# Kernel optimization log

Hardware: AMD Instinct MI355X
Metric: run time of the kernel (lower is better)

Reference implementation:

```python
import jax, jax.numpy as jnp
import numpy as np

HIDDEN = 1024
NUM_HEADS = 16
HEAD_DIM = HIDDEN // NUM_HEADS


def setup_inputs() -> dict:
    key = jax.random.key(0)
    ks = jax.random.split(key, 13)
    B, S, H = 4, 2048, HIDDEN
    sc = 1.0 / np.sqrt(H)
    inp = {
        'queries': jax.random.normal(ks[0], (B, S, H), jnp.float32),
        'keys': jax.random.normal(ks[1], (B, S, H), jnp.float32),
        'values': jax.random.normal(ks[2], (B, S, H), jnp.float32),
        'attention_mask': jax.random.randint(ks[3], (B, S, S), 0, 2, jnp.int32),
        'W_q': jax.random.normal(ks[4], (H, H), jnp.float32) * sc,
        'b_q': jnp.zeros((H,), jnp.float32),
        'W_k': jax.random.normal(ks[5], (H, H), jnp.float32) * sc,
        'b_k': jnp.zeros((H,), jnp.float32),
        'W_v': jax.random.normal(ks[6], (H, H), jnp.float32) * sc,
        'b_v': jnp.zeros((H,), jnp.float32),
        'W_o': jax.random.normal(ks[7], (H, H), jnp.float32) * sc,
        'b_o': jnp.zeros((H,), jnp.float32),
    }
    return inp


def _split_heads(x):
    # [B, S, H] -> [B, nH, S, d]
    B, S, _ = x.shape
    return x.reshape(B, S, NUM_HEADS, HEAD_DIM).transpose(0, 2, 1, 3)


def reference(queries, keys, values, attention_mask, W_q, b_q, W_k, b_k, W_v, b_v, W_o, b_o):
    q = _split_heads(queries @ W_q + b_q)   # [B, nH, S, d]
    k = _split_heads(keys @ W_k + b_k)
    v = _split_heads(values @ W_v + b_v)
    d = q.shape[-1]
    scores = jnp.einsum('bhqd,bhkd->bhqk', q, k) / jnp.sqrt(jnp.float32(d))
    # mask repeat_interleave over heads == broadcast mask over head axis
    mask = attention_mask[:, None, :, :]    # [B, 1, S, S]
    scores = jnp.where(mask == 0, jnp.float32(-1e6), scores)
    attn = jax.nn.softmax(scores, axis=-1)  # dropout p=0 -> identity
    out = jnp.einsum('bhqk,bhkd->bhqd', attn, v)  # [B, nH, S, d]
    B, _, S, _ = out.shape
    out = out.transpose(0, 2, 1, 3).reshape(B, S, NUM_HEADS * HEAD_DIM)
    return out @ W_o + b_o
```

## Files before the change

### kernel.cpp

```cpp
#include <hip/hip_runtime.h>
#include <stdint.h>

typedef unsigned short u16;
typedef uint32_t u32;
typedef unsigned long long u64;
typedef short bf16x8 __attribute__((ext_vector_type(8)));
typedef float f32x4 __attribute__((ext_vector_type(4)));
typedef float f32x16 __attribute__((ext_vector_type(16)));

#define MFMA16 __builtin_amdgcn_mfma_f32_16x16x32_bf16
#define MFMA32 __builtin_amdgcn_mfma_f32_32x32x16_bf16
#define L2E 1.44269504088896340736f

static __device__ __forceinline__ u16 f2bf(float f) {
  union { float f; u32 u; } v; v.f = f;
  u32 r = v.u + 0x7FFFu + ((v.u >> 16) & 1u);
  return (u16)(r >> 16);
}

static __device__ __forceinline__ u32 cvtpk(float lo, float hi) {
  u32 r;
  asm("v_cvt_pk_bf16_f32 %0, %1, %2" : "=v"(r) : "v"(lo), "v"(hi));
  return r;
}

static __device__ __forceinline__ void glds16(const u16* g, u16* l) {
  __builtin_amdgcn_global_load_lds((const __attribute__((address_space(1))) void*)g,
                                   (__attribute__((address_space(3))) void*)l, 16, 0, 0);
}

__global__ __launch_bounds__(256) void cvt3_kernel(
    const float* __restrict__ s0, const float* __restrict__ s1, const float* __restrict__ s2,
    u16* __restrict__ d0, u16* __restrict__ d1, u16* __restrict__ d2) {
  const float* s = (blockIdx.z == 0) ? s0 : (blockIdx.z == 1) ? s1 : s2;
  u16* d = (blockIdx.z == 0) ? d0 : (blockIdx.z == 1) ? d1 : d2;
  size_t i = ((size_t)blockIdx.x * 256 + threadIdx.x) * 8;
  float4 a = *(const float4*)(s + i);
  float4 c = *(const float4*)(s + i + 4);
  bf16x8 o;
  o[0] = (short)f2bf(a.x); o[1] = (short)f2bf(a.y);
  o[2] = (short)f2bf(a.z); o[3] = (short)f2bf(a.w);
  o[4] = (short)f2bf(c.x); o[5] = (short)f2bf(c.y);
  o[6] = (short)f2bf(c.z); o[7] = (short)f2bf(c.w);
  *(bf16x8*)(d + i) = o;
}

__global__ __launch_bounds__(256) void wtrans_kernel(
    const float* __restrict__ w0, const float* __restrict__ w1,
    const float* __restrict__ w2, const float* __restrict__ w3,
    u16* __restrict__ t0, u16* __restrict__ t1, u16* __restrict__ t2, u16* __restrict__ t3) {
  const float* w = (blockIdx.z == 0) ? w0 : (blockIdx.z == 1) ? w1 : (blockIdx.z == 2) ? w2 : w3;
  u16* t = (blockIdx.z == 0) ? t0 : (blockIdx.z == 1) ? t1 : (blockIdx.z == 2) ? t2 : t3;
  __shared__ float tile[64][65];
  const int bx = blockIdx.x, by = blockIdx.y;
#pragma unroll
  for (int i = 0; i < 16; ++i) {
    int idx = i * 256 + threadIdx.x;
    int r = idx >> 6, c = idx & 63;
    tile[r][c] = w[(size_t)(by * 64 + r) * 1024 + bx * 64 + c];
  }
  __syncthreads();
#pragma unroll
  for (int i = 0; i < 16; ++i) {
    int idx = i * 256 + threadIdx.x;
    int r = idx >> 6, c = idx & 63;
    t[(size_t)(bx * 64 + r) * 1024 + by * 64 + c] = f2bf(tile[c][r]);
  }
}

__global__ __launch_bounds__(256) void packmask_kernel(const int* __restrict__ m,
                                                       u32* __restrict__ pmo) {
  const size_t i = (size_t)blockIdx.x * 256 + threadIdx.x;
  const int lane = threadIdx.x & 63;
  unsigned long long b = __ballot(m[i] != 0);
  if (lane == 0) pmo[i >> 5] = (u32)b;
  else if (lane == 32) pmo[i >> 5] = (u32)(b >> 32);
}

template <int OM>
__global__ __launch_bounds__(256, 2) void gemm_kernel(
    const u16* __restrict__ A, const u16* __restrict__ Bt, const float* __restrict__ bias,
    void* __restrict__ Cout, float oscale) {
  constexpr int K = 1024, N = 1024;
  __shared__ u16 As[128 * 64];
  __shared__ u16 Bs[128 * 64];
  const int tid = threadIdx.x;
  const int lane = tid & 63;
  const int wid = tid >> 6;
  const int l15 = lane & 15;
  const int lg = lane >> 4;
  const int row0 = blockIdx.x * 128;
  const int col0 = blockIdx.y * 128;
  const int wr = wid >> 1, wc = wid & 1;
  const f32x4 fzero = {0.f, 0.f, 0.f, 0.f};

  f32x4 acc[4][4];
#pragma unroll
  for (int m = 0; m < 4; ++m)
#pragma unroll
    for (int n = 0; n < 4; ++n) acc[m][n] = fzero;

  for (int k0 = 0; k0 < K; k0 += 64) {
#pragma unroll
    for (int i = 0; i < 4; ++i) {
      int e = (i * 256 + tid) * 8;
      int r = e >> 6, c = e & 63;
      glds16(A + (size_t)(row0 + r) * K + k0 + c, As + (i * 256 + wid * 64) * 8);
      glds16(Bt + (size_t)(col0 + r) * K + k0 + c, Bs + (i * 256 + wid * 64) * 8);
    }
    __syncthreads();
#pragma unroll
    for (int ks = 0; ks < 2; ++ks) {
      const int koff = ks * 32 + lg * 8;
      bf16x8 af[4], bfr[4];
#pragma unroll
      for (int m = 0; m < 4; ++m)
        af[m] = *(const bf16x8*)(As + (wr * 64 + m * 16 + l15) * 64 + koff);
#pragma unroll
      for (int n = 0; n < 4; ++n)
        bfr[n] = *(const bf16x8*)(Bs + (wc * 64 + n * 16 + l15) * 64 + koff);
#pragma unroll
      for (int m = 0; m < 4; ++m)
#pragma unroll
        for (int n = 0; n < 4; ++n)
          acc[m][n] = MFMA16(af[m], bfr[n], acc[m][n], 0, 0, 0);
    }
    __syncthreads();
  }

#pragma unroll
  for (int n = 0; n < 4; ++n) {
    const int col = col0 + wc * 64 + n * 16 + l15;
    const float bv = bias[col];
#pragma unroll
    for (int m = 0; m < 4; ++m) {
#pragma unroll
      for (int r = 0; r < 4; ++r) {
        const int row = row0 + wr * 64 + m * 16 + lg * 4 + r;
        const float v = (acc[m][n][r] + bv) * oscale;
        if constexpr (OM == 0) {
          ((u16*)Cout)[(size_t)row * N + col] = f2bf(v);
        } else if constexpr (OM == 1) {
          ((float*)Cout)[(size_t)row * N + col] = v;
        } else {
          const int b_ = row >> 11, s_ = row & 2047, h_ = col >> 6, d_ = col & 63;
          ((u16*)Cout)[(size_t)((b_ * 16 + h_) * 64 + d_) * 2048 + s_] = f2bf(v);
        }
      }
    }
  }
}

__global__ __launch_bounds__(256, 4) void attn_kernel(
    const u16* __restrict__ Qb, const u16* __restrict__ Kb, const u16* __restrict__ Vt,
    const u32* __restrict__ pm, u16* __restrict__ Oa) {
  __shared__ u16 Ks[2][64 * 64];
  __shared__ u16 Vs[2][64 * 64];
  __shared__ uint4 mlut[16];
  const int tid = threadIdx.x;
  const int lane = tid & 63;
  const int wid = tid >> 6;
  const int c31 = lane & 31;
  const int hi = lane >> 5;
  const int qt = blockIdx.x;
  const int hh = blockIdx.y;
  const int bb = blockIdx.z;
  const int qbase = qt * 128 + wid * 32;
  const int sw = (lane & 7) << 3;

  if (tid < 16)
    mlut[tid] = make_uint4((u32) - (int)(tid & 1), (u32) - (int)((tid >> 1) & 1),
                           (u32) - (int)((tid >> 2) & 1), (u32) - (int)((tid >> 3) & 1));

  const size_t qrow = (size_t)(bb * 2048 + qbase + c31);
  bf16x8 qf[4];
#pragma unroll
  for (int ds = 0; ds < 4; ++ds)
    qf[ds] = *(const bf16x8*)(Qb + qrow * 1024 + hh * 64 + ds * 16 + hi * 8);

  float lrun = 0.f;
  f32x16 oacc[2];
#pragma unroll
  for (int dn = 0; dn < 2; ++dn)
#pragma unroll
    for (int r = 0; r < 16; ++r) oacc[dn][r] = 0.f;

  const size_t kgbase = (size_t)(bb * 2048) * 1024 + hh * 64;
  const size_t vgbase = (size_t)((bb * 16 + hh) * 64) * 2048;

#define STAGE(buf, kbase)                                                              \
  do {                                                                                 \
    _Pragma("unroll") for (int i = 0; i < 2; ++i) {                                    \
      int r = ((i * 256 + tid) * 8) >> 6, c = ((i * 256 + tid) * 8) & 63;              \
      int cs = c ^ ((r & 7) << 3);                                                     \
      glds16(Kb + kgbase + (size_t)((kbase) + r) * 1024 + cs,                          \
             &Ks[buf][(i * 256 + wid * 64) * 8]);                                      \
      glds16(Vt + vgbase + (size_t)r * 2048 + (kbase) + cs,                            \
             &Vs[buf][(i * 256 + wid * 64) * 8]);                                      \
    }                                                                                  \
  } while (0)

  STAGE(0, 0);
  __syncthreads();

  int cur = 0;
  for (int kt = 0; kt < 32; ++kt) {
    if (kt < 31) STAGE(cur ^ 1, (kt + 1) * 64);

    const u64 mw = *(const u64*)(pm + qrow * 64 + kt * 2);
    float ps = 0.f;

#pragma unroll
    for (int kb = 0; kb < 2; ++kb) {
      f32x16 sacc;
#pragma unroll
      for (int r = 0; r < 16; ++r) sacc[r] = 0.f;
#pragma unroll
      for (int ds = 0; ds < 4; ++ds) {
        bf16x8 kf = *(const bf16x8*)(&Ks[cur][(kb * 32 + c31) * 64 + ((ds * 16 + hi * 8) ^ sw)]);
        sacc = MFMA32(kf, qf[ds], sacc, 0, 0, 0);
      }

      const u32 mwk = (u32)(mw >> (kb * 32));
      u32 Ap[4], Bp[4];
#pragma unroll
      for (int q2 = 0; q2 < 4; ++q2) {
        const u32 kb4 = (mwk >> (q2 * 8 + hi * 4)) & 0xFu;
        const uint4 mm = mlut[kb4];
        const float p0 = __builtin_amdgcn_exp2f(sacc[4 * q2 + 0]);
        const float p1 = __builtin_amdgcn_exp2f(sacc[4 * q2 + 1]);
        const float p2 = __builtin_amdgcn_exp2f(sacc[4 * q2 + 2]);
        const float p3 = __builtin_amdgcn_exp2f(sacc[4 * q2 + 3]);
        const float f0 = __uint_as_float(__float_as_uint(p0) & mm.x);
        const float f1 = __uint_as_float(__float_as_uint(p1) & mm.y);
        const float f2 = __uint_as_float(__float_as_uint(p2) & mm.z);
        const float f3 = __uint_as_float(__float_as_uint(p3) & mm.w);
        ps += (f0 + f1) + (f2 + f3);
        Ap[q2] = cvtpk(f0, f1);
        Bp[q2] = cvtpk(f2, f3);
      }

      asm("v_permlane32_swap_b32 %0, %1" : "+v"(Ap[0]), "+v"(Ap[1]));
      asm("v_permlane32_swap_b32 %0, %1" : "+v"(Bp[0]), "+v"(Bp[1]));
      asm("v_permlane32_swap_b32 %0, %1" : "+v"(Ap[2]), "+v"(Ap[3]));
      asm("v_permlane32_swap_b32 %0, %1" : "+v"(Bp[2]), "+v"(Bp[3]));

#pragma unroll
      for (int t = 0; t < 2; ++t) {
        uint4 fr;
        fr.x = Ap[2 * t]; fr.y = Bp[2 * t]; fr.z = Ap[2 * t + 1]; fr.w = Bp[2 * t + 1];
        const bf16x8 pf = *(const bf16x8*)&fr;
        const int koff = (kb * 2 + t) * 16 + hi * 8;
#pragma unroll
        for (int dn = 0; dn < 2; ++dn) {
          bf16x8 vf = *(const bf16x8*)(&Vs[cur][(dn * 32 + c31) * 64 + (koff ^ sw)]);
          oacc[dn] = MFMA32(vf, pf, oacc[dn], 0, 0, 0);
        }
      }
    }

    ps += __shfl_xor(ps, 32);
    lrun += ps;

    __syncthreads();
    cur ^= 1;
  }
#undef STAGE

  const float inv = 1.0f / lrun;
  u16* orow = Oa + qrow * 1024 + hh * 64;
#pragma unroll
  for (int dn = 0; dn < 2; ++dn) {
#pragma unroll
    for (int q2 = 0; q2 < 4; ++q2) {
      uint2 w;
      w.x = cvtpk(oacc[dn][4 * q2 + 0] * inv, oacc[dn][4 * q2 + 1] * inv);
      w.y = cvtpk(oacc[dn][4 * q2 + 2] * inv, oacc[dn][4 * q2 + 3] * inv);
      *(uint2*)(orow + dn * 32 + q2 * 8 + hi * 4) = w;
    }
  }
}

extern "C" void kernel_launch(void* const* d_in, const int* in_sizes, int n_in,
                              void* d_out, int out_size, void* d_ws, size_t ws_size,
                              hipStream_t stream) {
  const float* q = (const float*)d_in[0];
  const float* k = (const float*)d_in[1];
  const float* v = (const float*)d_in[2];
  const int* mask = (const int*)d_in[3];
  const float* Wq = (const float*)d_in[4]; const float* bq = (const float*)d_in[5];
  const float* Wk = (const float*)d_in[6]; const float* bk = (const float*)d_in[7];
  const float* Wv = (const float*)d_in[8]; const float* bv = (const float*)d_in[9];
  const float* Wo = (const float*)d_in[10]; const float* bo = (const float*)d_in[11];
  float* out = (float*)d_out;
  char* ws = (char*)d_ws;
  const size_t MB = 1024ull * 1024ull;
  u16* qbf = (u16*)(ws + 0 * MB);
  u16* kbf = (u16*)(ws + 16 * MB);
  u16* vbf = (u16*)(ws + 32 * MB);
  u16* Qp  = (u16*)(ws + 48 * MB);
  u16* Kp  = (u16*)(ws + 64 * MB);
  u16* Vtp = (u16*)(ws + 80 * MB);
  u16* Wqt = (u16*)(ws + 96 * MB);
  u16* Wkt = (u16*)(ws + 98 * MB);
  u16* Wvt = (u16*)(ws + 100 * MB);
  u16* Wot = (u16*)(ws + 102 * MB);
  u32* pmb = (u32*)(ws + 104 * MB);
  u16* Oa  = qbf;

  const float QSCALE = 0.125f * L2E;

  cvt3_kernel<<<dim3(4096, 1, 3), 256, 0, stream>>>(q, k, v, qbf, kbf, vbf);
  wtrans_kernel<<<dim3(16, 16, 4), 256, 0, stream>>>(Wq, Wk, Wv, Wo, Wqt, Wkt, Wvt, Wot);
  packmask_kernel<<<dim3(65536), 256, 0, stream>>>(mask, pmb);
  gemm_kernel<0><<<dim3(64, 8), 256, 0, stream>>>(qbf, Wqt, bq, Qp, QSCALE);
  gemm_kernel<0><<<dim3(64, 8), 256, 0, stream>>>(kbf, Wkt, bk, Kp, 1.0f);
  gemm_kernel<2><<<dim3(64, 8), 256, 0, stream>>>(vbf, Wvt, bv, Vtp, 1.0f);
  attn_kernel<<<dim3(16, 16, 4), 256, 0, stream>>>(Qp, Kp, Vtp, pmb, Oa);
  gemm_kernel<1><<<dim3(64, 8), 256, 0, stream>>>(Oa, Wot, bo, out, 1.0f);
}
```

Measured before the change: 277.3 us.

## Triple-buffer GEMM with swizzled LDS and larger 256x128 tiles

```diff
diff --git a/kernel.cpp b/kernel.cpp
--- a/kernel.cpp
+++ b/kernel.cpp
@@ -78,20 +78,22 @@
 }
 
 template <int OM>
-__global__ __launch_bounds__(256, 2) void gemm_kernel(
+__global__ __launch_bounds__(512, 2) void gemm_kernel(
     const u16* __restrict__ A, const u16* __restrict__ Bt, const float* __restrict__ bias,
     void* __restrict__ Cout, float oscale) {
   constexpr int K = 1024, N = 1024;
-  __shared__ u16 As[128 * 64];
-  __shared__ u16 Bs[128 * 64];
+  constexpr int NT = K / 64;
+  __shared__ u16 As[3][256 * 64];
+  __shared__ u16 Bs[3][128 * 64];
   const int tid = threadIdx.x;
   const int lane = tid & 63;
   const int wid = tid >> 6;
   const int l15 = lane & 15;
   const int lg = lane >> 4;
-  const int row0 = blockIdx.x * 128;
+  const int row0 = blockIdx.x * 256;
   const int col0 = blockIdx.y * 128;
   const int wr = wid >> 1, wc = wid & 1;
+  const int swf = (l15 & 7) << 3;
   const f32x4 fzero = {0.f, 0.f, 0.f, 0.f};
 
   f32x4 acc[4][4];
@@ -100,33 +102,61 @@
 #pragma unroll
     for (int n = 0; n < 4; ++n) acc[m][n] = fzero;
 
-  for (int k0 = 0; k0 < K; k0 += 64) {
-#pragma unroll
-    for (int i = 0; i < 4; ++i) {
-      int e = (i * 256 + tid) * 8;
-      int r = e >> 6, c = e & 63;
-      glds16(A + (size_t)(row0 + r) * K + k0 + c, As + (i * 256 + wid * 64) * 8);
-      glds16(Bt + (size_t)(col0 + r) * K + k0 + c, Bs + (i * 256 + wid * 64) * 8);
-    }
-    __syncthreads();
+#define GSTAGE(buf, k0)                                                        \
+  do {                                                                         \
+    _Pragma("unroll") for (int i = 0; i < 4; ++i) {                            \
+      int e = (i * 512 + tid) * 8;                                             \
+      int r = e >> 6, c = e & 63;                                              \
+      int cs = c ^ ((r & 7) << 3);                                             \
+      glds16(A + (size_t)(row0 + r) * K + (k0) + cs, &As[buf][e]);             \
+    }                                                                          \
+    _Pragma("unroll") for (int i = 0; i < 2; ++i) {                            \
+      int e = (i * 512 + tid) * 8;                                             \
+      int r = e >> 6, c = e & 63;                                              \
+      int cs = c ^ ((r & 7) << 3);                                             \
+      glds16(Bt + (size_t)(col0 + r) * K + (k0) + cs, &Bs[buf][e]);            \
+    }                                                                          \
+  } while (0)
+
+  GSTAGE(0, 0);
+  GSTAGE(1, 64);
+  asm volatile("s_waitcnt vmcnt(6)" ::: "memory");
+  __builtin_amdgcn_s_barrier();
+  __builtin_amdgcn_sched_barrier(0);
+
+  for (int t = 0; t < NT; ++t) {
+    const int buf = t % 3;
+    if (t + 2 < NT) GSTAGE((t + 2) % 3, (t + 2) * 64);
+
+    __builtin_amdgcn_s_setprio(1);
 #pragma unroll
     for (int ks = 0; ks < 2; ++ks) {
       const int koff = ks * 32 + lg * 8;
       bf16x8 af[4], bfr[4];
 #pragma unroll
       for (int m = 0; m < 4; ++m)
-        af[m] = *(const bf16x8*)(As + (wr * 64 + m * 16 + l15) * 64 + koff);
+        af[m] = *(const bf16x8*)(&As[buf][(wr * 64 + m * 16 + l15) * 64 + (koff ^ swf)]);
 #pragma unroll
       for (int n = 0; n < 4; ++n)
-        bfr[n] = *(const bf16x8*)(Bs + (wc * 64 + n * 16 + l15) * 64 + koff);
+        bfr[n] = *(const bf16x8*)(&Bs[buf][(wc * 64 + n * 16 + l15) * 64 + (koff ^ swf)]);
 #pragma unroll
       for (int m = 0; m < 4; ++m)
 #pragma unroll
         for (int n = 0; n < 4; ++n)
           acc[m][n] = MFMA16(af[m], bfr[n], acc[m][n], 0, 0, 0);
     }
-    __syncthreads();
-  }
+    __builtin_amdgcn_s_setprio(0);
+
+    if (t + 1 < NT) {
+      if (t + 2 < NT)
+        asm volatile("s_waitcnt vmcnt(6)" ::: "memory");
+      else
+        asm volatile("s_waitcnt vmcnt(0)" ::: "memory");
+      __builtin_amdgcn_s_barrier();
+      __builtin_amdgcn_sched_barrier(0);
+    }
+  }
+#undef GSTAGE
 
 #pragma unroll
   for (int n = 0; n < 4; ++n) {
@@ -313,9 +343,9 @@
   cvt3_kernel<<<dim3(4096, 1, 3), 256, 0, stream>>>(q, k, v, qbf, kbf, vbf);
   wtrans_kernel<<<dim3(16, 16, 4), 256, 0, stream>>>(Wq, Wk, Wv, Wo, Wqt, Wkt, Wvt, Wot);
   packmask_kernel<<<dim3(65536), 256, 0, stream>>>(mask, pmb);
-  gemm_kernel<0><<<dim3(64, 8), 256, 0, stream>>>(qbf, Wqt, bq, Qp, QSCALE);
-  gemm_kernel<0><<<dim3(64, 8), 256, 0, stream>>>(kbf, Wkt, bk, Kp, 1.0f);
-  gemm_kernel<2><<<dim3(64, 8), 256, 0, stream>>>(vbf, Wvt, bv, Vtp, 1.0f);
+  gemm_kernel<0><<<dim3(32, 8), 512, 0, stream>>>(qbf, Wqt, bq, Qp, QSCALE);
+  gemm_kernel<0><<<dim3(32, 8), 512, 0, stream>>>(kbf, Wkt, bk, Kp, 1.0f);
+  gemm_kernel<2><<<dim3(32, 8), 512, 0, stream>>>(vbf, Wvt, bv, Vtp, 1.0f);
   attn_kernel<<<dim3(16, 16, 4), 256, 0, stream>>>(Qp, Kp, Vtp, pmb, Oa);
-  gemm_kernel<1><<<dim3(64, 8), 256, 0, stream>>>(Oa, Wot, bo, out, 1.0f);
-}
+  gemm_kernel<1><<<dim3(32, 8), 512, 0, stream>>>(Oa, Wot, bo, out, 1.0f);
+}
```

After: 267.6 us. 3.5% less time.
